# Optimization experiments

Measured on AMD Instinct MI355X. Metric: run time of the kernel, lower is better.

Reference implementation:

```python
import jax, jax.numpy as jnp
import numpy as np

# SpargeAttn / spas_sage2_attn_meansim block sizes
BLKQ, BLKK = 128, 64
NUM_HEADS = 8
SIMTHRESHD1 = 0.6
CDFTHRESHD = 0.98


def _block_meta(t, blk):
    # t: [B,H,S,D] -> block means [B,H,nb,D] and min-cosine-to-mean per block [B,H,nb]
    B, H, S, D = t.shape
    nb = S // blk
    tb = t.reshape(B, H, nb, blk, D)
    m = tb.mean(axis=3)
    tn = tb / (jnp.linalg.norm(tb, axis=-1, keepdims=True) + 1e-6)
    mn = m / (jnp.linalg.norm(m, axis=-1, keepdims=True) + 1e-6)
    cos = jnp.einsum('bhnkd,bhnd->bhnk', tn, mn)
    return m, cos.min(axis=-1)


def _meansim_sparse_attention(q, k, v, scale):
    # Block-sparse attention with mean-similarity pruning (SpargeAttn meansim).
    qm, qsim = _block_meta(q, BLKQ)          # [B,H,nq,D], [B,H,nq]
    km, ksim = _block_meta(k, BLKK)          # [B,H,nk,D], [B,H,nk]
    q_self = qsim > SIMTHRESHD1              # self-similar Q blocks -> mean is representative
    k_self = ksim > SIMTHRESHD1
    # pooled attention map over block means
    pooled = jax.nn.softmax(jnp.einsum('bhqd,bhkd->bhqk', qm, km) * scale, axis=-1)
    # per Q-block row: keep highest-prob K blocks until cumulative mass >= cdfthreshd
    order = jnp.argsort(-pooled, axis=-1)
    sp = jnp.take_along_axis(pooled, order, axis=-1)
    csum = jnp.cumsum(sp, axis=-1)
    keep_sorted = (csum - sp) < CDFTHRESHD   # always keeps at least the top block
    inv = jnp.argsort(order, axis=-1)
    keep = jnp.take_along_axis(keep_sorted, inv, axis=-1)  # [B,H,nq,nk]
    # conservative fallback: non-self-similar Q/K blocks are never pruned
    block_mask = keep | (~q_self)[..., None] | (~k_self)[:, :, None, :]
    tok_mask = jnp.repeat(jnp.repeat(block_mask, BLKQ, axis=2), BLKK, axis=3)
    s = jnp.einsum('bhqd,bhkd->bhqk', q, k) * scale
    s = jnp.where(tok_mask, s, -jnp.inf)
    p = jax.nn.softmax(s, axis=-1)
    return jnp.einsum('bhqk,bhkd->bhqd', p, v)


def setup_inputs() -> dict:
    key = jax.random.key(0)
    B, L, C = 2, 2048, 512
    ks = jax.random.split(key, 3)
    x = jax.random.normal(ks[0], (B, L, C), jnp.float32)
    Wqkv = jax.random.normal(ks[1], (C, 3 * C), jnp.float32) * (C ** -0.5)
    bqkv = jnp.zeros((3 * C,), jnp.float32)
    Wproj = jax.random.normal(ks[2], (C, C), jnp.float32) * (C ** -0.5)
    bproj = jnp.zeros((C,), jnp.float32)
    return {"x": x, "Wqkv": Wqkv, "bqkv": bqkv, "Wproj": Wproj, "bproj": bproj}


def reference(x, Wqkv, bqkv, Wproj, bproj):
    B, L, C = x.shape
    H = NUM_HEADS
    D = C // H
    scale = D ** -0.5
    qkv = (x @ Wqkv + bqkv).reshape(B, L, 3, H, D)
    qkv = jnp.transpose(qkv, (2, 0, 3, 1, 4))  # [3,B,H,L,D]
    q, k, v = qkv[0], qkv[1], qkv[2]
    o = _meansim_sparse_attention(q, k, v, scale)  # [B,H,L,D]
    o = jnp.transpose(o, (0, 2, 1, 3)).reshape(B, L, C)
    return o @ Wproj + bproj
```

## Files before the change

### kernel.cpp

```cpp
#include <hip/hip_runtime.h>
#include <math.h>

typedef unsigned short ushortT;
typedef unsigned int uintT;
typedef __attribute__((ext_vector_type(8))) short short8;
typedef __attribute__((ext_vector_type(16))) float f32x16;
#define MFMA32(a, b, c) __builtin_amdgcn_mfma_f32_32x32x16_bf16((a), (b), (c), 0, 0, 0)


#define LOG2E 1.4426950408889634f

static __device__ __forceinline__ ushortT f2b(float f) {
    union { float f; uintT u; } v; v.f = f;
    uintT u = v.u;
    u += 0x7fffu + ((u >> 16) & 1u);
    return (ushortT)(u >> 16);
}
static __device__ __forceinline__ uintT pack2(float a, float b) {
    return (uintT)f2b(a) | ((uintT)f2b(b) << 16);
}
static __device__ __forceinline__ uintT pack2t(float a, float b) {
    union { float f; uintT u; } x0, x1; x0.f = a; x1.f = b;
    return __builtin_amdgcn_perm(x1.u, x0.u, 0x07060302u);
}
static __device__ __forceinline__ float blo(uintT u) {
    union { uintT u; float f; } v; v.u = u << 16; return v.f;
}
static __device__ __forceinline__ float bhi(uintT u) {
    union { uintT u; float f; } v; v.u = u & 0xffff0000u; return v.f;
}
static __device__ __forceinline__ f32x16 zero16() {
    f32x16 z;
    #pragma unroll
    for (int i = 0; i < 16; ++i) z[i] = 0.f;
    return z;
}

#define B_N 2
#define H_N 8
#define L_N 2048
#define NQB 16
#define NKB 32

__global__ __launch_bounds__(256) void prep_kernel(
    const float* __restrict__ x, ushortT* __restrict__ xb,
    const float* __restrict__ Wq, ushortT* __restrict__ Wqt,
    const float* __restrict__ Wp, ushortT* __restrict__ Wpt) {
    const int bid = blockIdx.x, t = threadIdx.x;
    __shared__ float tile[32][33];
    if (bid < 2048) {
        int i = (bid * 256 + t) * 4;
        float4 v = *(const float4*)(x + i);
        uint2 o; o.x = pack2(v.x, v.y); o.y = pack2(v.z, v.w);
        *(uint2*)(xb + i) = o;
        return;
    }
    const float* W; ushortT* Wt; int C, c0, r0;
    if (bid < 2816) {
        const int b = bid - 2048;
        W = Wq; Wt = Wqt; C = 1536;
        c0 = (b % 48) * 32; r0 = (b / 48) * 32;
    } else {
        const int b = bid - 2816;
        W = Wp; Wt = Wpt; C = 512;
        c0 = (b & 15) * 32; r0 = (b >> 4) * 32;
    }
    const int tx = t & 31, ty = t >> 5;
    #pragma unroll
    for (int i = 0; i < 4; ++i)
        tile[ty + 8 * i][tx] = W[(size_t)(r0 + ty + 8 * i) * C + c0 + tx];
    __syncthreads();
    #pragma unroll
    for (int i = 0; i < 4; ++i) {
        int rr = ty + 8 * i;
        Wt[(size_t)(c0 + rr) * 512 + r0 + tx] = f2b(tile[tx][rr]);
    }
}

__global__ __launch_bounds__(256) void qkv_gemm_kernel(
    const ushortT* __restrict__ xb, const ushortT* __restrict__ wt,
    const float* __restrict__ bias,
    ushortT* __restrict__ qb, ushortT* __restrict__ kbuf, ushortT* __restrict__ vt,
    float* __restrict__ qm, float* __restrict__ km) {
    __shared__ __align__(16) ushortT As[2][128 * 40];
    __shared__ __align__(16) ushortT Bs[2][64 * 40];
    __shared__ float sumbuf[4][64];
    const int t = threadIdx.x;
    const int l = t & 63, w = t >> 6;
    const int lm = l & 31, lh = l >> 5;
    const int rowbase = blockIdx.y * 128;
    const int colbase = blockIdx.x * 64;

    f32x16 acc[2];
    acc[0] = zero16(); acc[1] = zero16();

    const int r = t >> 1, half = t & 1;
    const ushortT* Ag = xb + (size_t)(rowbase + r) * 512 + half * 16;
    const int soA = r * 40 + half * 16;
    const int rb = t >> 2, q4 = t & 3;
    const ushortT* Bg = wt + (size_t)(colbase + rb) * 512 + q4 * 8;
    const int soB = rb * 40 + q4 * 8;

    uint4 a0, a1, b0;
    a0 = *(const uint4*)(Ag); a1 = *(const uint4*)(Ag + 8);
    b0 = *(const uint4*)(Bg);
    *(uint4*)(&As[0][soA]) = a0; *(uint4*)(&As[0][soA] + 8) = a1;
    *(uint4*)(&Bs[0][soB]) = b0;

    for (int k0 = 0; k0 < 512; k0 += 32) {
        const int cur = (k0 >> 5) & 1;
        __syncthreads();
        if (k0 < 480) {
            a0 = *(const uint4*)(Ag + k0 + 32); a1 = *(const uint4*)(Ag + k0 + 40);
            b0 = *(const uint4*)(Bg + k0 + 32);
        }
        #pragma unroll
        for (int ks = 0; ks < 2; ++ks) {
            const int ko = 16 * ks + 8 * lh;
            short8 af  = *(const short8*)(&As[cur][(32 * w + lm) * 40 + ko]);
            short8 b_0 = *(const short8*)(&Bs[cur][lm * 40 + ko]);
            short8 b_1 = *(const short8*)(&Bs[cur][(32 + lm) * 40 + ko]);
            acc[0] = MFMA32(af, b_0, acc[0]);
            acc[1] = MFMA32(af, b_1, acc[1]);
        }
        if (k0 < 480) {
            const int nxt = cur ^ 1;
            *(uint4*)(&As[nxt][soA]) = a0; *(uint4*)(&As[nxt][soA] + 8) = a1;
            *(uint4*)(&Bs[nxt][soB]) = b0;
        }
    }

    const int which = blockIdx.x >> 3;
    const int h = blockIdx.x & 7;
    const int by = blockIdx.y;
    const int b = by >> 4;
    const size_t hb = (size_t)(b * 8 + h);
    float bias2[2];
    #pragma unroll
    for (int nt = 0; nt < 2; ++nt) bias2[nt] = bias[colbase + 32 * nt + lm];
    float msum[2] = {0.f, 0.f};
    #pragma unroll
    for (int nt = 0; nt < 2; ++nt) {
        const int dd = 32 * nt + lm;
        #pragma unroll
        for (int rg = 0; rg < 16; ++rg) {
            const int row_local = 32 * w + (rg & 3) + 8 * (rg >> 2) + 4 * lh;
            const int ll = (rowbase + row_local) & 2047;
            float val = acc[nt][rg] + bias2[nt];
            if (which == 0) {
                val *= 0.125f;
                msum[nt] += val;
                qb[(hb * 2048 + ll) * 64 + dd] = f2b(val * LOG2E);
            } else if (which == 1) {
                msum[nt] += val;
                kbuf[(hb * 2048 + ll) * 64 + dd] = f2b(val);
            } else {
                vt[hb * 131072 + (size_t)(ll >> 6) * 4096 + dd * 64 + (ll & 63)] = f2b(val);
            }
        }
    }
    if (which == 2) return;
    #pragma unroll
    for (int nt = 0; nt < 2; ++nt) {
        float s = msum[nt] + __shfl_xor(msum[nt], 32);
        if (l < 32) sumbuf[w][32 * nt + lm] = s;
    }
    __syncthreads();
    if (which == 0) {
        if (t < 64) {
            const int qbi = by & 15;
            qm[(hb * 16 + qbi) * 64 + t] =
                (sumbuf[0][t] + sumbuf[1][t] + sumbuf[2][t] + sumbuf[3][t]) * (1.0f / 128.0f);
        }
    } else {
        if (t < 128) {
            const int d = t & 63, pair = t >> 6;
            const int kbi = 2 * (by & 15) + pair;
            km[(hb * 32 + kbi) * 64 + d] =
                (sumbuf[2 * pair][d] + sumbuf[2 * pair + 1][d]) * (1.0f / 64.0f);
        }
    }
}

__global__ __launch_bounds__(256) void cos_kernel(const ushortT* __restrict__ qb,
                                                  const ushortT* __restrict__ kbuf,
                                                  const float* __restrict__ qm,
                                                  const float* __restrict__ km,
                                                  float* __restrict__ qs,
                                                  float* __restrict__ ks) {
    const int bh = blockIdx.y, t = threadIdx.x;
    const int l = t & 63, w = t >> 6;
    __shared__ float mS[64];
    __shared__ float wmin[4];
    if (blockIdx.z == 0) {
        if (blockIdx.x >= 16) return;
        const int qbk = blockIdx.x;
        if (t < 64) mS[t] = qm[((size_t)bh * 16 + qbk) * 64 + t];
        __syncthreads();
        float qn = 0.f;
        #pragma unroll
        for (int d = 0; d < 64; ++d) qn += mS[d] * mS[d];
        qn = sqrtf(qn);
        const int tok = t >> 1, half = t & 1;
        const ushortT* qrow = qb + ((size_t)bh * 2048 + qbk * 128 + tok) * 64 + half * 32;
        float dot = 0.f, nn = 0.f;
        #pragma unroll
        for (int c = 0; c < 4; ++c) {
            uint4 u = *(const uint4*)(qrow + c * 8);
            const int db = half * 32 + c * 8;
            float f0 = blo(u.x), f1 = bhi(u.x), f2 = blo(u.y), f3 = bhi(u.y);
            float f4 = blo(u.z), f5 = bhi(u.z), f6 = blo(u.w), f7 = bhi(u.w);
            dot += f0 * mS[db] + f1 * mS[db + 1] + f2 * mS[db + 2] + f3 * mS[db + 3]
                 + f4 * mS[db + 4] + f5 * mS[db + 5] + f6 * mS[db + 6] + f7 * mS[db + 7];
            nn += f0 * f0 + f1 * f1 + f2 * f2 + f3 * f3 + f4 * f4 + f5 * f5 + f6 * f6 + f7 * f7;
        }
        dot += __shfl_xor(dot, 1);
        nn += __shfl_xor(nn, 1);
        float cosv = dot / ((sqrtf(nn) + 1e-6f) * (qn + 1e-6f));
        #pragma unroll
        for (int off = 1; off < 64; off <<= 1) cosv = fminf(cosv, __shfl_xor(cosv, off));
        if (l == 0) wmin[w] = cosv;
        __syncthreads();
        if (t == 0)
            qs[bh * 16 + qbk] = fminf(fminf(wmin[0], wmin[1]), fminf(wmin[2], wmin[3]));
    } else {
        const int kbk = blockIdx.x;
        if (t < 64) mS[t] = km[((size_t)bh * 32 + kbk) * 64 + t];
        __syncthreads();
        float kn = 0.f;
        #pragma unroll
        for (int d = 0; d < 64; ++d) kn += mS[d] * mS[d];
        kn = sqrtf(kn);
        const int tok = t >> 2, quarter = t & 3;
        const ushortT* krow = kbuf + ((size_t)bh * 2048 + kbk * 64 + tok) * 64 + quarter * 16;
        float dot = 0.f, nn = 0.f;
        #pragma unroll
        for (int c = 0; c < 2; ++c) {
            uint4 u = *(const uint4*)(krow + c * 8);
            const int db = quarter * 16 + c * 8;
            float f0 = blo(u.x), f1 = bhi(u.x), f2 = blo(u.y), f3 = bhi(u.y);
            float f4 = blo(u.z), f5 = bhi(u.z), f6 = blo(u.w), f7 = bhi(u.w);
            dot += f0 * mS[db] + f1 * mS[db + 1] + f2 * mS[db + 2] + f3 * mS[db + 3]
                 + f4 * mS[db + 4] + f5 * mS[db + 5] + f6 * mS[db + 6] + f7 * mS[db + 7];
            nn += f0 * f0 + f1 * f1 + f2 * f2 + f3 * f3 + f4 * f4 + f5 * f5 + f6 * f6 + f7 * f7;
        }
        dot += __shfl_xor(dot, 1); dot += __shfl_xor(dot, 2);
        nn += __shfl_xor(nn, 1); nn += __shfl_xor(nn, 2);
        float cosv = dot / ((sqrtf(nn) + 1e-6f) * (kn + 1e-6f));
        #pragma unroll
        for (int off = 1; off < 64; off <<= 1) cosv = fminf(cosv, __shfl_xor(cosv, off));
        if (l == 0) wmin[w] = cosv;
        __syncthreads();
        if (t == 0)
            ks[bh * 32 + kbk] = fminf(fminf(wmin[0], wmin[1]), fminf(wmin[2], wmin[3]));
    }
}

__global__ __launch_bounds__(512) void mask_kernel(const float* __restrict__ qm,
                                                   const float* __restrict__ km,
                                                   const float* __restrict__ qs,
                                                   const float* __restrict__ ks,
                                                   int* __restrict__ maskp) {
    const int bh = blockIdx.x, t = threadIdx.x;
    __shared__ float qmS[16 * 64];
    __shared__ float kmS[32 * 64];
    __shared__ float pooled[16 * 32];
    __shared__ float pnorm[16 * 32];
    for (int i = t; i < 1024; i += 512) qmS[i] = qm[(size_t)bh * 1024 + i];
    for (int i = t; i < 2048; i += 512) kmS[i] = km[(size_t)bh * 2048 + i];
    __syncthreads();
    {
        const int qbi = t >> 5, kbi = t & 31;
        float dot = 0.f;
        #pragma unroll
        for (int d = 0; d < 64; ++d) dot += qmS[qbi * 64 + d] * kmS[kbi * 64 + d];
        pooled[t] = dot;
    }
    __syncthreads();
    if (t < 16) {
        float mx = -1e30f;
        #pragma unroll
        for (int kb = 0; kb < NKB; ++kb) mx = fmaxf(mx, pooled[t * 32 + kb]);
        float sum = 0.f;
        #pragma unroll
        for (int kb = 0; kb < NKB; ++kb) {
            const float e = expf(pooled[t * 32 + kb] - mx);
            pnorm[t * 32 + kb] = e;
            sum += e;
        }
        const float inv = 1.0f / sum;
        #pragma unroll
        for (int kb = 0; kb < NKB; ++kb) pnorm[t * 32 + kb] *= inv;
    }
    __syncthreads();
    {
        const int row = t >> 5, kb = t & 31;
        const float pk = pnorm[row * 32 + kb];
        float before = 0.f;
        #pragma unroll
        for (int j = 0; j < NKB; ++j) {
            const float pj = pnorm[row * 32 + j];
            if (pj > pk || (pj == pk && j < kb)) before += pj;
        }
        const bool keep = before < 0.98f;
        const bool qfb = !(qs[bh * 16 + row] > 0.6f);
        const bool kfb = !(ks[bh * 32 + kb] > 0.6f);
        maskp[((size_t)bh * 16 + row) * 32 + kb] = (keep || qfb || kfb) ? 1 : 0;
    }
}

#define KS_SH (128 * 72)
#define VS_SH (64 * 136)
__global__ __launch_bounds__(512, 2) void attn_kernel(
    const ushortT* __restrict__ qb, const ushortT* __restrict__ kbuf,
    const ushortT* __restrict__ vt, const int* __restrict__ maskp,
    ushortT* __restrict__ ob) {
    __shared__ __align__(16) ushortT smem[2 * KS_SH + 2 * VS_SH];
    __shared__ int klist[33];
    ushortT (*Ks)[KS_SH] = (ushortT(*)[KS_SH])smem;
    ushortT (*Vs)[VS_SH] = (ushortT(*)[VS_SH])(smem + 2 * KS_SH);

    const int t = threadIdx.x;
    const int l = t & 63, w = t >> 6;
    const int lm = l & 31, lh = l >> 5;
    const int qc = w >> 2, kq = w & 3;
    const int bh = blockIdx.x, qt = blockIdx.y;

    if (w == 0) {
        const int* mrow = maskp + ((size_t)bh * 16 + qt) * 32;
        const int keep = (l < 32) ? mrow[l] : 0;
        unsigned long long bal = __ballot(keep != 0);
        if (keep) {
            const int rank = __popcll(bal & ((1ULL << l) - 1ULL));
            klist[rank] = l;
        }
        if (l == 0) klist[32] = __popcll(bal);
    }
    const ushortT* qg = qb + ((size_t)bh * 2048 + qt * 128) * 64;
    short8 qf[4][2];
    #pragma unroll
    for (int qh = 0; qh < 2; ++qh)
        #pragma unroll
        for (int ksd = 0; ksd < 4; ++ksd)
            qf[ksd][qh] = *(const short8*)(qg + (64 * qc + 32 * qh + lm) * 64 + 16 * ksd + 8 * lh);
    __syncthreads();

    const int cnt = klist[32];
    const int nIter = (cnt + 1) >> 1;

    const int tile = t >> 7, tt = t & 127;
    const int isV = tile >> 1, skh = tile & 1;
    const int srow = tt >> 1, shalf = (tt & 1) * 32;
    const ushortT* gsrc = (isV ? vt : kbuf) + (size_t)bh * 131072;
    const int goff = srow * 64 + shalf;
    const int soff = isV ? (srow * 136 + skh * 64 + shalf)
                         : ((skh * 64 + srow) * 72 + shalf);
    ushortT* sd0 = (isV ? &Vs[0][soff] : &Ks[0][soff]);
    ushortT* sd1 = (isV ? &Vs[1][soff] : &Ks[1][soff]);

    f32x16 oacc[2][2];
    oacc[0][0] = zero16(); oacc[1][0] = zero16();
    oacc[0][1] = zero16(); oacc[1][1] = zero16();
    float l_i[2] = {0.f, 0.f};

    uint4 st0, st1, st2, st3;
    {
        int kidx = skh; if (kidx >= cnt) kidx = cnt - 1;
        const ushortT* g = gsrc + (size_t)klist[kidx] * 4096 + goff;
        st0 = *(const uint4*)(g);      st1 = *(const uint4*)(g + 8);
        st2 = *(const uint4*)(g + 16); st3 = *(const uint4*)(g + 24);
        *(uint4*)(sd0)      = st0; *(uint4*)(sd0 + 8)  = st1;
        *(uint4*)(sd0 + 16) = st2; *(uint4*)(sd0 + 24) = st3;
    }

    for (int i = 0; i < nIter; ++i) {
        const int cur = i & 1;
        __syncthreads();
        if (i + 1 < nIter) {
            int kidx = 2 * (i + 1) + skh; if (kidx >= cnt) kidx = cnt - 1;
            const ushortT* g = gsrc + (size_t)klist[kidx] * 4096 + goff;
            st0 = *(const uint4*)(g);      st1 = *(const uint4*)(g + 8);
            st2 = *(const uint4*)(g + 16); st3 = *(const uint4*)(g + 24);
        }
        const float mf = (2 * i + (kq >> 1) < cnt) ? 1.f : 0.f;
        f32x16 sacc[2];
        sacc[0] = zero16(); sacc[1] = zero16();
        #pragma unroll
        for (int ksd = 0; ksd < 4; ++ksd) {
            const int ko = 16 * ksd + 8 * lh;
            short8 kf = *(const short8*)(&Ks[cur][(32 * kq + lm) * 72 + ko]);
            sacc[0] = MFMA32(kf, qf[ksd][0], sacc[0]);
            sacc[1] = MFMA32(kf, qf[ksd][1], sacc[1]);
        }
        uintT uu[2][4][2];
        #pragma unroll
        for (int qh = 0; qh < 2; ++qh) {
            float psum0 = 0.f, psum1 = 0.f;
            #pragma unroll
            for (int rp = 0; rp < 8; ++rp) {
                const float e0 = __builtin_amdgcn_exp2f(sacc[qh][2 * rp]) * mf;
                const float e1 = __builtin_amdgcn_exp2f(sacc[qh][2 * rp + 1]) * mf;
                psum0 += e0; psum1 += e1;
                uu[qh][rp >> 1][rp & 1] = pack2t(e0, e1);
            }
            float psum = psum0 + psum1;
            psum += __shfl_xor(psum, 32);
            l_i[qh] += psum;
        }
        #pragma unroll
        for (int ksk = 0; ksk < 2; ++ksk) {
            const int vko = 32 * kq + 16 * ksk + 8 * lh;
            short8 vf0 = *(const short8*)(&Vs[cur][lm * 136 + vko]);
            short8 vf1 = *(const short8*)(&Vs[cur][(32 + lm) * 136 + vko]);
            #pragma unroll
            for (int qh = 0; qh < 2; ++qh) {
                const uintT kA = lh ? uu[qh][2 * ksk + 1][0] : uu[qh][2 * ksk][0];
                const uintT kB = lh ? uu[qh][2 * ksk + 1][1] : uu[qh][2 * ksk][1];
                const uintT sA = lh ? uu[qh][2 * ksk][0] : uu[qh][2 * ksk + 1][0];
                const uintT sB = lh ? uu[qh][2 * ksk][1] : uu[qh][2 * ksk + 1][1];
                const uintT rA = (uintT)__shfl_xor((int)sA, 32);
                const uintT rB = (uintT)__shfl_xor((int)sB, 32);
                union { uintT u[4]; short8 v; } cv;
                if (lh == 0) { cv.u[0] = kA; cv.u[1] = kB; cv.u[2] = rA; cv.u[3] = rB; }
                else         { cv.u[0] = rA; cv.u[1] = rB; cv.u[2] = kA; cv.u[3] = kB; }
                oacc[0][qh] = MFMA32(vf0, cv.v, oacc[0][qh]);
                oacc[1][qh] = MFMA32(vf1, cv.v, oacc[1][qh]);
            }
        }
        if (i + 1 < nIter) {
            ushortT* sd = (cur ^ 1) ? sd1 : sd0;
            *(uint4*)(sd)      = st0; *(uint4*)(sd + 8)  = st1;
            *(uint4*)(sd + 16) = st2; *(uint4*)(sd + 24) = st3;
        }
    }

    uint4* ox = (uint4*)smem;
    float* lx = (float*)((char*)smem + 49152);
    __syncthreads();
    if (kq != 0) {
        const int wslot = qc * 3 + (kq - 1);
        #pragma unroll
        for (int dt = 0; dt < 2; ++dt)
            #pragma unroll
            for (int qh = 0; qh < 2; ++qh)
                #pragma unroll
                for (int g2 = 0; g2 < 2; ++g2) {
                    uint4 u;
                    u.x = pack2(oacc[dt][qh][8 * g2 + 0], oacc[dt][qh][8 * g2 + 1]);
                    u.y = pack2(oacc[dt][qh][8 * g2 + 2], oacc[dt][qh][8 * g2 + 3]);
                    u.z = pack2(oacc[dt][qh][8 * g2 + 4], oacc[dt][qh][8 * g2 + 5]);
                    u.w = pack2(oacc[dt][qh][8 * g2 + 6], oacc[dt][qh][8 * g2 + 7]);
                    ox[(wslot * 8 + (dt * 4 + qh * 2 + g2)) * 64 + l] = u;
                }
        if (lh == 0) {
            lx[(wslot * 2 + 0) * 32 + lm] = l_i[0];
            lx[(wslot * 2 + 1) * 32 + lm] = l_i[1];
        }
    }
    __syncthreads();
    if (kq == 0) {
        float lt[2] = {l_i[0], l_i[1]};
        #pragma unroll
        for (int p = 0; p < 3; ++p) {
            const int ws2 = qc * 3 + p;
            lt[0] += lx[(ws2 * 2 + 0) * 32 + lm];
            lt[1] += lx[(ws2 * 2 + 1) * 32 + lm];
            #pragma unroll
            for (int dt = 0; dt < 2; ++dt)
                #pragma unroll
                for (int qh = 0; qh < 2; ++qh)
                    #pragma unroll
                    for (int g2 = 0; g2 < 2; ++g2) {
                        uint4 u = ox[(ws2 * 8 + (dt * 4 + qh * 2 + g2)) * 64 + l];
                        oacc[dt][qh][8 * g2 + 0] += blo(u.x);
                        oacc[dt][qh][8 * g2 + 1] += bhi(u.x);
                        oacc[dt][qh][8 * g2 + 2] += blo(u.y);
                        oacc[dt][qh][8 * g2 + 3] += bhi(u.y);
                        oacc[dt][qh][8 * g2 + 4] += blo(u.z);
                        oacc[dt][qh][8 * g2 + 5] += bhi(u.z);
                        oacc[dt][qh][8 * g2 + 6] += blo(u.w);
                        oacc[dt][qh][8 * g2 + 7] += bhi(u.w);
                    }
        }
        #pragma unroll
        for (int qh = 0; qh < 2; ++qh) {
            const float inv = 1.0f / lt[qh];
            const int token = qt * 128 + qc * 64 + 32 * qh + lm;
            ushortT* orow = ob + ((size_t)bh * 2048 + token) * 64;
            #pragma unroll
            for (int dt = 0; dt < 2; ++dt)
                #pragma unroll
                for (int rp = 0; rp < 8; ++rp) {
                    const int d0 = 32 * dt + 8 * (rp >> 1) + 4 * lh + 2 * (rp & 1);
                    *(uintT*)(orow + d0) =
                        pack2(oacc[dt][qh][2 * rp] * inv, oacc[dt][qh][2 * rp + 1] * inv);
                }
        }
    }
}

__global__ __launch_bounds__(256) void proj_gemm_kernel(
    const ushortT* __restrict__ ob, const ushortT* __restrict__ wpt,
    const float* __restrict__ bias, float* __restrict__ out) {
    __shared__ __align__(16) ushortT As[2][64 * 40];
    __shared__ __align__(16) ushortT Bs[2][64 * 40];
    const int t = threadIdx.x;
    const int l = t & 63, w = t >> 6;
    const int lm = l & 31, lh = l >> 5;
    const int rh = w & 1, ch = w >> 1;
    const int rowbase = blockIdx.y * 64;
    const int colbase = blockIdx.x * 64;

    f32x16 acc = zero16();

    const int r = t >> 2, q4 = t & 3;
    const int token = rowbase + r;
    const int b2 = token >> 11, lt = token & 2047;
    const int so = r * 40 + q4 * 8;
    const ushortT* obbase = ob + ((size_t)(b2 * 8) * 2048 + lt) * 64 + q4 * 8;
    const ushortT* Bg = wpt + (size_t)(colbase + r) * 512 + q4 * 8;

    uint4 a0, b0;
    a0 = *(const uint4*)(obbase);
    b0 = *(const uint4*)(Bg);
    *(uint4*)(&As[0][so]) = a0;
    *(uint4*)(&Bs[0][so]) = b0;

    for (int k0 = 0; k0 < 512; k0 += 32) {
        const int cur = (k0 >> 5) & 1;
        __syncthreads();
        if (k0 < 480) {
            const int kn = k0 + 32;
            const ushortT* Ag = obbase + (size_t)(kn >> 6) * 131072 + (kn & 63);
            a0 = *(const uint4*)(Ag);
            b0 = *(const uint4*)(Bg + kn);
        }
        #pragma unroll
        for (int ks = 0; ks < 2; ++ks) {
            const int ko = 16 * ks + 8 * lh;
            short8 af = *(const short8*)(&As[cur][(32 * rh + lm) * 40 + ko]);
            short8 bf = *(const short8*)(&Bs[cur][(32 * ch + lm) * 40 + ko]);
            acc = MFMA32(af, bf, acc);
        }
        if (k0 < 480) {
            const int nxt = cur ^ 1;
            *(uint4*)(&As[nxt][so]) = a0;
            *(uint4*)(&Bs[nxt][so]) = b0;
        }
    }
    const int c = colbase + 32 * ch + lm;
    const float bb = bias[c];
    #pragma unroll
    for (int rg = 0; rg < 16; ++rg) {
        const int row_local = 32 * rh + (rg & 3) + 8 * (rg >> 2) + 4 * lh;
        out[(size_t)(rowbase + row_local) * 512 + c] = acc[rg] + bb;
    }
}

extern "C" void kernel_launch(void* const* d_in, const int* in_sizes, int n_in,
                              void* d_out, int out_size, void* d_ws, size_t ws_size,
                              hipStream_t stream) {
    const float* x     = (const float*)d_in[0];
    const float* Wqkv  = (const float*)d_in[1];
    const float* bqkv  = (const float*)d_in[2];
    const float* Wproj = (const float*)d_in[3];
    const float* bproj = (const float*)d_in[4];
    float* out = (float*)d_out;

    char* w = (char*)d_ws;
    ushortT* xb     = (ushortT*)(w);
    ushortT* wqkvt  = (ushortT*)(w + 4194304);
    ushortT* wprojt = (ushortT*)(w + 5767168);
    ushortT* qb     = (ushortT*)(w + 6291456);
    ushortT* kbuf   = (ushortT*)(w + 10485760);
    ushortT* vt     = (ushortT*)(w + 14680064);
    ushortT* ob     = (ushortT*)(w + 18874368);
    float*   qm     = (float*)(w + 23068672);
    float*   km     = (float*)(w + 23134208);
    int*     maskp  = (int*)(w + 23265280);
    float*   qs     = (float*)(w + 36406272);
    float*   ks     = (float*)(w + 36407296);

    prep_kernel<<<3072, 256, 0, stream>>>(x, xb, Wqkv, wqkvt, Wproj, wprojt);
    qkv_gemm_kernel<<<dim3(24, 32), 256, 0, stream>>>(xb, wqkvt, bqkv, qb, kbuf, vt, qm, km);
    cos_kernel<<<dim3(32, 16, 2), 256, 0, stream>>>(qb, kbuf, qm, km, qs, ks);
    mask_kernel<<<16, 512, 0, stream>>>(qm, km, qs, ks, maskp);
    attn_kernel<<<dim3(16, 16), 512, 0, stream>>>(qb, kbuf, vt, maskp, ob);
    proj_gemm_kernel<<<dim3(8, 64), 256, 0, stream>>>(ob, wprojt, bproj, out);
}
```

Measured before the change: 141.3 us.

## Drop LDS staging of K/V in attention; each wave reads its K blocks from global

Removes the double-buffered shared-memory staging of K and V tiles and the per-iteration block-wide barrier. Each wave now takes a strided subset of the kept K blocks (j = kq, kq+4, ...) and loads its K and V MFMA fragments straight from global memory, processing both 32-row halves of each 64-key block itself. This drops LDS traffic and synchronisation and shrinks shared memory to the reduction buffers, but fragment loads now come uncoalesced from global/L2 with no prefetch overlap, and work may be unbalanced across waves when the kept-block count is not a multiple of four.

```diff
diff --git a/kernel.cpp b/kernel.cpp
--- a/kernel.cpp
+++ b/kernel.cpp
@@ -309,16 +309,13 @@
     }
 }
 
-#define KS_SH (128 * 72)
-#define VS_SH (64 * 136)
 __global__ __launch_bounds__(512, 2) void attn_kernel(
     const ushortT* __restrict__ qb, const ushortT* __restrict__ kbuf,
     const ushortT* __restrict__ vt, const int* __restrict__ maskp,
     ushortT* __restrict__ ob) {
-    __shared__ __align__(16) ushortT smem[2 * KS_SH + 2 * VS_SH];
+    __shared__ __align__(16) uint4 ox[6 * 8 * 64];
+    __shared__ float lx[6 * 2 * 32];
     __shared__ int klist[33];
-    ushortT (*Ks)[KS_SH] = (ushortT(*)[KS_SH])smem;
-    ushortT (*Vs)[VS_SH] = (ushortT(*)[VS_SH])(smem + 2 * KS_SH);
 
     const int t = threadIdx.x;
     const int l = t & 63, w = t >> 6;
@@ -346,97 +343,66 @@
     __syncthreads();
 
     const int cnt = klist[32];
-    const int nIter = (cnt + 1) >> 1;
-
-    const int tile = t >> 7, tt = t & 127;
-    const int isV = tile >> 1, skh = tile & 1;
-    const int srow = tt >> 1, shalf = (tt & 1) * 32;
-    const ushortT* gsrc = (isV ? vt : kbuf) + (size_t)bh * 131072;
-    const int goff = srow * 64 + shalf;
-    const int soff = isV ? (srow * 136 + skh * 64 + shalf)
-                         : ((skh * 64 + srow) * 72 + shalf);
-    ushortT* sd0 = (isV ? &Vs[0][soff] : &Ks[0][soff]);
-    ushortT* sd1 = (isV ? &Vs[1][soff] : &Ks[1][soff]);
+    const ushortT* kgb = kbuf + (size_t)bh * 131072;
+    const ushortT* vgb = vt + (size_t)bh * 131072;
 
     f32x16 oacc[2][2];
     oacc[0][0] = zero16(); oacc[1][0] = zero16();
     oacc[0][1] = zero16(); oacc[1][1] = zero16();
     float l_i[2] = {0.f, 0.f};
 
-    uint4 st0, st1, st2, st3;
-    {
-        int kidx = skh; if (kidx >= cnt) kidx = cnt - 1;
-        const ushortT* g = gsrc + (size_t)klist[kidx] * 4096 + goff;
-        st0 = *(const uint4*)(g);      st1 = *(const uint4*)(g + 8);
-        st2 = *(const uint4*)(g + 16); st3 = *(const uint4*)(g + 24);
-        *(uint4*)(sd0)      = st0; *(uint4*)(sd0 + 8)  = st1;
-        *(uint4*)(sd0 + 16) = st2; *(uint4*)(sd0 + 24) = st3;
-    }
-
-    for (int i = 0; i < nIter; ++i) {
-        const int cur = i & 1;
-        __syncthreads();
-        if (i + 1 < nIter) {
-            int kidx = 2 * (i + 1) + skh; if (kidx >= cnt) kidx = cnt - 1;
-            const ushortT* g = gsrc + (size_t)klist[kidx] * 4096 + goff;
-            st0 = *(const uint4*)(g);      st1 = *(const uint4*)(g + 8);
-            st2 = *(const uint4*)(g + 16); st3 = *(const uint4*)(g + 24);
-        }
-        const float mf = (2 * i + (kq >> 1) < cnt) ? 1.f : 0.f;
-        f32x16 sacc[2];
-        sacc[0] = zero16(); sacc[1] = zero16();
-        #pragma unroll
-        for (int ksd = 0; ksd < 4; ++ksd) {
-            const int ko = 16 * ksd + 8 * lh;
-            short8 kf = *(const short8*)(&Ks[cur][(32 * kq + lm) * 72 + ko]);
-            sacc[0] = MFMA32(kf, qf[ksd][0], sacc[0]);
-            sacc[1] = MFMA32(kf, qf[ksd][1], sacc[1]);
-        }
-        uintT uu[2][4][2];
-        #pragma unroll
-        for (int qh = 0; qh < 2; ++qh) {
-            float psum0 = 0.f, psum1 = 0.f;
+    for (int j = kq; j < cnt; j += 4) {
+        const int kb = klist[j];
+        const ushortT* kg = kgb + (size_t)kb * 4096;
+        const ushortT* vg = vgb + (size_t)kb * 4096;
+        #pragma unroll
+        for (int kh = 0; kh < 2; ++kh) {
+            f32x16 sacc[2];
+            sacc[0] = zero16(); sacc[1] = zero16();
             #pragma unroll
-            for (int rp = 0; rp < 8; ++rp) {
-                const float e0 = __builtin_amdgcn_exp2f(sacc[qh][2 * rp]) * mf;
-                const float e1 = __builtin_amdgcn_exp2f(sacc[qh][2 * rp + 1]) * mf;
-                psum0 += e0; psum1 += e1;
-                uu[qh][rp >> 1][rp & 1] = pack2t(e0, e1);
+            for (int ksd = 0; ksd < 4; ++ksd) {
+                short8 kf = *(const short8*)(kg + (32 * kh + lm) * 64 + 16 * ksd + 8 * lh);
+                sacc[0] = MFMA32(kf, qf[ksd][0], sacc[0]);
+                sacc[1] = MFMA32(kf, qf[ksd][1], sacc[1]);
             }
-            float psum = psum0 + psum1;
-            psum += __shfl_xor(psum, 32);
-            l_i[qh] += psum;
-        }
-        #pragma unroll
-        for (int ksk = 0; ksk < 2; ++ksk) {
-            const int vko = 32 * kq + 16 * ksk + 8 * lh;
-            short8 vf0 = *(const short8*)(&Vs[cur][lm * 136 + vko]);
-            short8 vf1 = *(const short8*)(&Vs[cur][(32 + lm) * 136 + vko]);
+            uintT uu[2][4][2];
             #pragma unroll
             for (int qh = 0; qh < 2; ++qh) {
-                const uintT kA = lh ? uu[qh][2 * ksk + 1][0] : uu[qh][2 * ksk][0];
-                const uintT kB = lh ? uu[qh][2 * ksk + 1][1] : uu[qh][2 * ksk][1];
-                const uintT sA = lh ? uu[qh][2 * ksk][0] : uu[qh][2 * ksk + 1][0];
-                const uintT sB = lh ? uu[qh][2 * ksk][1] : uu[qh][2 * ksk + 1][1];
-                const uintT rA = (uintT)__shfl_xor((int)sA, 32);
-                const uintT rB = (uintT)__shfl_xor((int)sB, 32);
-                union { uintT u[4]; short8 v; } cv;
-                if (lh == 0) { cv.u[0] = kA; cv.u[1] = kB; cv.u[2] = rA; cv.u[3] = rB; }
-                else         { cv.u[0] = rA; cv.u[1] = rB; cv.u[2] = kA; cv.u[3] = kB; }
-                oacc[0][qh] = MFMA32(vf0, cv.v, oacc[0][qh]);
-                oacc[1][qh] = MFMA32(vf1, cv.v, oacc[1][qh]);
+                float psum0 = 0.f, psum1 = 0.f;
+                #pragma unroll
+                for (int rp = 0; rp < 8; ++rp) {
+                    const float e0 = __builtin_amdgcn_exp2f(sacc[qh][2 * rp]);
+                    const float e1 = __builtin_amdgcn_exp2f(sacc[qh][2 * rp + 1]);
+                    psum0 += e0; psum1 += e1;
+                    uu[qh][rp >> 1][rp & 1] = pack2t(e0, e1);
+                }
+                float psum = psum0 + psum1;
+                psum += __shfl_xor(psum, 32);
+                l_i[qh] += psum;
             }
-        }
-        if (i + 1 < nIter) {
-            ushortT* sd = (cur ^ 1) ? sd1 : sd0;
-            *(uint4*)(sd)      = st0; *(uint4*)(sd + 8)  = st1;
-            *(uint4*)(sd + 16) = st2; *(uint4*)(sd + 24) = st3;
-        }
-    }
-
-    uint4* ox = (uint4*)smem;
-    float* lx = (float*)((char*)smem + 49152);
-    __syncthreads();
+            #pragma unroll
+            for (int ksk = 0; ksk < 2; ++ksk) {
+                const int vko = 32 * kh + 16 * ksk + 8 * lh;
+                short8 vf0 = *(const short8*)(vg + lm * 64 + vko);
+                short8 vf1 = *(const short8*)(vg + (32 + lm) * 64 + vko);
+                #pragma unroll
+                for (int qh = 0; qh < 2; ++qh) {
+                    const uintT kA = lh ? uu[qh][2 * ksk + 1][0] : uu[qh][2 * ksk][0];
+                    const uintT kB = lh ? uu[qh][2 * ksk + 1][1] : uu[qh][2 * ksk][1];
+                    const uintT sA = lh ? uu[qh][2 * ksk][0] : uu[qh][2 * ksk + 1][0];
+                    const uintT sB = lh ? uu[qh][2 * ksk][1] : uu[qh][2 * ksk + 1][1];
+                    const uintT rA = (uintT)__shfl_xor((int)sA, 32);
+                    const uintT rB = (uintT)__shfl_xor((int)sB, 32);
+                    union { uintT u[4]; short8 v; } cv;
+                    if (lh == 0) { cv.u[0] = kA; cv.u[1] = kB; cv.u[2] = rA; cv.u[3] = rB; }
+                    else         { cv.u[0] = rA; cv.u[1] = rB; cv.u[2] = kA; cv.u[3] = kB; }
+                    oacc[0][qh] = MFMA32(vf0, cv.v, oacc[0][qh]);
+                    oacc[1][qh] = MFMA32(vf1, cv.v, oacc[1][qh]);
+                }
+            }
+        }
+    }
+
     if (kq != 0) {
         const int wslot = qc * 3 + (kq - 1);
         #pragma unroll
```

Result: slower. 149.9 us (+6.1%).

## Fuse cosine-similarity into QKV GEMM epilogue and mask into attention prologue

Applied to the files above, without the earlier changes.

The per-block min-cosine computation moves into the QKV GEMM epilogue, working on the fp32 accumulators already in registers. This removes the separate cos_kernel launch and its reread of Q/K from memory. The pooled softmax, CDF pruning and mask building move into the attention kernel prologue, one row per workgroup, which removes mask_kernel and the mask buffer. The cost is two fewer launches and less global traffic, traded for extra shuffle reductions in the GEMM epilogue and a small serial prologue in attention. Cosines now use unrounded fp32 values instead of bf16, which could flip threshold decisions slightly.

```diff
diff --git a/kernel.cpp b/kernel.cpp
--- a/kernel.cpp
+++ b/kernel.cpp
@@ -81,10 +81,13 @@
     const ushortT* __restrict__ xb, const ushortT* __restrict__ wt,
     const float* __restrict__ bias,
     ushortT* __restrict__ qb, ushortT* __restrict__ kbuf, ushortT* __restrict__ vt,
-    float* __restrict__ qm, float* __restrict__ km) {
+    float* __restrict__ qm, float* __restrict__ km,
+    float* __restrict__ qs, float* __restrict__ ks) {
     __shared__ __align__(16) ushortT As[2][128 * 40];
     __shared__ __align__(16) ushortT Bs[2][64 * 40];
     __shared__ float sumbuf[4][64];
+    __shared__ float meanS[2][64];
+    __shared__ float wminS[4];
     const int t = threadIdx.x;
     const int l = t & 63, w = t >> 6;
     const int lm = l & 31, lh = l >> 5;
@@ -115,8 +118,8 @@
             b0 = *(const uint4*)(Bg + k0 + 32);
         }
         #pragma unroll
-        for (int ks = 0; ks < 2; ++ks) {
-            const int ko = 16 * ks + 8 * lh;
+        for (int ks2 = 0; ks2 < 2; ++ks2) {
+            const int ko = 16 * ks2 + 8 * lh;
             short8 af  = *(const short8*)(&As[cur][(32 * w + lm) * 40 + ko]);
             short8 b_0 = *(const short8*)(&Bs[cur][lm * 40 + ko]);
             short8 b_1 = *(const short8*)(&Bs[cur][(32 + lm) * 40 + ko]);
@@ -157,6 +160,7 @@
             } else {
                 vt[hb * 131072 + (size_t)(ll >> 6) * 4096 + dd * 64 + (ll & 63)] = f2b(val);
             }
+            acc[nt][rg] = val;
         }
     }
     if (which == 2) return;
@@ -169,143 +173,54 @@
     if (which == 0) {
         if (t < 64) {
             const int qbi = by & 15;
-            qm[(hb * 16 + qbi) * 64 + t] =
+            const float m =
                 (sumbuf[0][t] + sumbuf[1][t] + sumbuf[2][t] + sumbuf[3][t]) * (1.0f / 128.0f);
+            qm[(hb * 16 + qbi) * 64 + t] = m;
+            meanS[0][t] = m;
         }
     } else {
         if (t < 128) {
             const int d = t & 63, pair = t >> 6;
             const int kbi = 2 * (by & 15) + pair;
-            km[(hb * 32 + kbi) * 64 + d] =
+            const float m =
                 (sumbuf[2 * pair][d] + sumbuf[2 * pair + 1][d]) * (1.0f / 64.0f);
-        }
-    }
-}
-
-__global__ __launch_bounds__(256) void cos_kernel(const ushortT* __restrict__ qb,
-                                                  const ushortT* __restrict__ kbuf,
-                                                  const float* __restrict__ qm,
-                                                  const float* __restrict__ km,
-                                                  float* __restrict__ qs,
-                                                  float* __restrict__ ks) {
-    const int bh = blockIdx.y, t = threadIdx.x;
-    const int l = t & 63, w = t >> 6;
-    __shared__ float mS[64];
-    __shared__ float wmin[4];
-    if (blockIdx.z == 0) {
-        if (blockIdx.x >= 16) return;
-        const int qbk = blockIdx.x;
-        if (t < 64) mS[t] = qm[((size_t)bh * 16 + qbk) * 64 + t];
-        __syncthreads();
-        float qn = 0.f;
-        #pragma unroll
-        for (int d = 0; d < 64; ++d) qn += mS[d] * mS[d];
-        qn = sqrtf(qn);
-        const int tok = t >> 1, half = t & 1;
-        const ushortT* qrow = qb + ((size_t)bh * 2048 + qbk * 128 + tok) * 64 + half * 32;
-        float dot = 0.f, nn = 0.f;
-        #pragma unroll
-        for (int c = 0; c < 4; ++c) {
-            uint4 u = *(const uint4*)(qrow + c * 8);
-            const int db = half * 32 + c * 8;
-            float f0 = blo(u.x), f1 = bhi(u.x), f2 = blo(u.y), f3 = bhi(u.y);
-            float f4 = blo(u.z), f5 = bhi(u.z), f6 = blo(u.w), f7 = bhi(u.w);
-            dot += f0 * mS[db] + f1 * mS[db + 1] + f2 * mS[db + 2] + f3 * mS[db + 3]
-                 + f4 * mS[db + 4] + f5 * mS[db + 5] + f6 * mS[db + 6] + f7 * mS[db + 7];
-            nn += f0 * f0 + f1 * f1 + f2 * f2 + f3 * f3 + f4 * f4 + f5 * f5 + f6 * f6 + f7 * f7;
-        }
-        dot += __shfl_xor(dot, 1);
-        nn += __shfl_xor(nn, 1);
-        float cosv = dot / ((sqrtf(nn) + 1e-6f) * (qn + 1e-6f));
-        #pragma unroll
-        for (int off = 1; off < 64; off <<= 1) cosv = fminf(cosv, __shfl_xor(cosv, off));
-        if (l == 0) wmin[w] = cosv;
-        __syncthreads();
-        if (t == 0)
-            qs[bh * 16 + qbk] = fminf(fminf(wmin[0], wmin[1]), fminf(wmin[2], wmin[3]));
-    } else {
-        const int kbk = blockIdx.x;
-        if (t < 64) mS[t] = km[((size_t)bh * 32 + kbk) * 64 + t];
-        __syncthreads();
-        float kn = 0.f;
-        #pragma unroll
-        for (int d = 0; d < 64; ++d) kn += mS[d] * mS[d];
-        kn = sqrtf(kn);
-        const int tok = t >> 2, quarter = t & 3;
-        const ushortT* krow = kbuf + ((size_t)bh * 2048 + kbk * 64 + tok) * 64 + quarter * 16;
-        float dot = 0.f, nn = 0.f;
-        #pragma unroll
-        for (int c = 0; c < 2; ++c) {
-            uint4 u = *(const uint4*)(krow + c * 8);
-            const int db = quarter * 16 + c * 8;
-            float f0 = blo(u.x), f1 = bhi(u.x), f2 = blo(u.y), f3 = bhi(u.y);
-            float f4 = blo(u.z), f5 = bhi(u.z), f6 = blo(u.w), f7 = bhi(u.w);
-            dot += f0 * mS[db] + f1 * mS[db + 1] + f2 * mS[db + 2] + f3 * mS[db + 3]
-                 + f4 * mS[db + 4] + f5 * mS[db + 5] + f6 * mS[db + 6] + f7 * mS[db + 7];
-            nn += f0 * f0 + f1 * f1 + f2 * f2 + f3 * f3 + f4 * f4 + f5 * f5 + f6 * f6 + f7 * f7;
-        }
-        dot += __shfl_xor(dot, 1); dot += __shfl_xor(dot, 2);
-        nn += __shfl_xor(nn, 1); nn += __shfl_xor(nn, 2);
-        float cosv = dot / ((sqrtf(nn) + 1e-6f) * (kn + 1e-6f));
-        #pragma unroll
-        for (int off = 1; off < 64; off <<= 1) cosv = fminf(cosv, __shfl_xor(cosv, off));
-        if (l == 0) wmin[w] = cosv;
-        __syncthreads();
-        if (t == 0)
-            ks[bh * 32 + kbk] = fminf(fminf(wmin[0], wmin[1]), fminf(wmin[2], wmin[3]));
-    }
-}
-
-__global__ __launch_bounds__(512) void mask_kernel(const float* __restrict__ qm,
-                                                   const float* __restrict__ km,
-                                                   const float* __restrict__ qs,
-                                                   const float* __restrict__ ks,
-                                                   int* __restrict__ maskp) {
-    const int bh = blockIdx.x, t = threadIdx.x;
-    __shared__ float qmS[16 * 64];
-    __shared__ float kmS[32 * 64];
-    __shared__ float pooled[16 * 32];
-    __shared__ float pnorm[16 * 32];
-    for (int i = t; i < 1024; i += 512) qmS[i] = qm[(size_t)bh * 1024 + i];
-    for (int i = t; i < 2048; i += 512) kmS[i] = km[(size_t)bh * 2048 + i];
+            km[(hb * 32 + kbi) * 64 + d] = m;
+            meanS[pair][d] = m;
+        }
+    }
     __syncthreads();
     {
-        const int qbi = t >> 5, kbi = t & 31;
-        float dot = 0.f;
-        #pragma unroll
-        for (int d = 0; d < 64; ++d) dot += qmS[qbi * 64 + d] * kmS[kbi * 64 + d];
-        pooled[t] = dot;
-    }
-    __syncthreads();
-    if (t < 16) {
-        float mx = -1e30f;
-        #pragma unroll
-        for (int kb = 0; kb < NKB; ++kb) mx = fmaxf(mx, pooled[t * 32 + kb]);
-        float sum = 0.f;
-        #pragma unroll
-        for (int kb = 0; kb < NKB; ++kb) {
-            const float e = expf(pooled[t * 32 + kb] - mx);
-            pnorm[t * 32 + kb] = e;
-            sum += e;
-        }
-        const float inv = 1.0f / sum;
-        #pragma unroll
-        for (int kb = 0; kb < NKB; ++kb) pnorm[t * 32 + kb] *= inv;
-    }
-    __syncthreads();
-    {
-        const int row = t >> 5, kb = t & 31;
-        const float pk = pnorm[row * 32 + kb];
-        float before = 0.f;
-        #pragma unroll
-        for (int j = 0; j < NKB; ++j) {
-            const float pj = pnorm[row * 32 + j];
-            if (pj > pk || (pj == pk && j < kb)) before += pj;
-        }
-        const bool keep = before < 0.98f;
-        const bool qfb = !(qs[bh * 16 + row] > 0.6f);
-        const bool kfb = !(ks[bh * 32 + kb] > 0.6f);
-        maskp[((size_t)bh * 16 + row) * 32 + kb] = (keep || qfb || kfb) ? 1 : 0;
+        const int mrow = (which == 0) ? 0 : (w >> 1);
+        const float mv0 = meanS[mrow][lm], mv1 = meanS[mrow][32 + lm];
+        float mn2 = mv0 * mv0 + mv1 * mv1;
+        #pragma unroll
+        for (int off = 1; off < 32; off <<= 1) mn2 += __shfl_xor(mn2, off);
+        const float mnorm = sqrtf(mn2);
+        float cmin = 1e30f;
+        #pragma unroll
+        for (int rg = 0; rg < 16; ++rg) {
+            float dp = acc[0][rg] * mv0 + acc[1][rg] * mv1;
+            float nn = acc[0][rg] * acc[0][rg] + acc[1][rg] * acc[1][rg];
+            #pragma unroll
+            for (int off = 1; off < 32; off <<= 1) {
+                dp += __shfl_xor(dp, off);
+                nn += __shfl_xor(nn, off);
+            }
+            const float cosv = dp / ((sqrtf(nn) + 1e-6f) * (mnorm + 1e-6f));
+            cmin = fminf(cmin, cosv);
+        }
+        cmin = fminf(cmin, __shfl_xor(cmin, 32));
+        if (l == 0) wminS[w] = cmin;
+    }
+    __syncthreads();
+    if (t == 0) {
+        if (which == 0) {
+            qs[hb * 16 + (by & 15)] =
+                fminf(fminf(wminS[0], wminS[1]), fminf(wminS[2], wminS[3]));
+        } else {
+            ks[hb * 32 + 2 * (by & 15)]     = fminf(wminS[0], wminS[1]);
+            ks[hb * 32 + 2 * (by & 15) + 1] = fminf(wminS[2], wminS[3]);
+        }
     }
 }
 
@@ -313,10 +228,14 @@
 #define VS_SH (64 * 136)
 __global__ __launch_bounds__(512, 2) void attn_kernel(
     const ushortT* __restrict__ qb, const ushortT* __restrict__ kbuf,
-    const ushortT* __restrict__ vt, const int* __restrict__ maskp,
+    const ushortT* __restrict__ vt,
+    const float* __restrict__ qm, const float* __restrict__ km,
+    const float* __restrict__ qs, const float* __restrict__ ks,
     ushortT* __restrict__ ob) {
     __shared__ __align__(16) ushortT smem[2 * KS_SH + 2 * VS_SH];
     __shared__ int klist[33];
+    __shared__ float qmS[64];
+    __shared__ float pnS[32];
     ushortT (*Ks)[KS_SH] = (ushortT(*)[KS_SH])smem;
     ushortT (*Vs)[VS_SH] = (ushortT(*)[VS_SH])(smem + 2 * KS_SH);
 
@@ -326,23 +245,47 @@
     const int qc = w >> 2, kq = w & 3;
     const int bh = blockIdx.x, qt = blockIdx.y;
 
-    if (w == 0) {
-        const int* mrow = maskp + ((size_t)bh * 16 + qt) * 32;
-        const int keep = (l < 32) ? mrow[l] : 0;
-        unsigned long long bal = __ballot(keep != 0);
+    if (t < 64) qmS[t] = qm[((size_t)bh * 16 + qt) * 64 + t];
+
+    const ushortT* qg = qb + ((size_t)bh * 2048 + qt * 128) * 64;
+    short8 qf[4][2];
+    #pragma unroll
+    for (int qh = 0; qh < 2; ++qh)
+        #pragma unroll
+        for (int ksd = 0; ksd < 4; ++ksd)
+            qf[ksd][qh] = *(const short8*)(qg + (64 * qc + 32 * qh + lm) * 64 + 16 * ksd + 8 * lh);
+    __syncthreads();
+
+    if (w == 0 && l < 32) {
+        const float* kmr = km + ((size_t)bh * 32 + l) * 64;
+        float dot = 0.f;
+        #pragma unroll
+        for (int d = 0; d < 64; ++d) dot += qmS[d] * kmr[d];
+        float mx = dot;
+        #pragma unroll
+        for (int off = 1; off < 32; off <<= 1) mx = fmaxf(mx, __shfl_xor(mx, off));
+        const float e = expf(dot - mx);
+        float sum = e;
+        #pragma unroll
+        for (int off = 1; off < 32; off <<= 1) sum += __shfl_xor(sum, off);
+        const float pn = e * (1.0f / sum);
+        pnS[l] = pn;
+        float before = 0.f;
+        #pragma unroll
+        for (int j = 0; j < 32; ++j) {
+            const float pj = pnS[j];
+            if (pj > pn || (pj == pn && j < l)) before += pj;
+        }
+        const bool qfb = !(qs[bh * 16 + qt] > 0.6f);
+        const bool kfb = !(ks[bh * 32 + l] > 0.6f);
+        const bool keep = (before < 0.98f) || qfb || kfb;
+        unsigned long long bal = __ballot(keep);
         if (keep) {
             const int rank = __popcll(bal & ((1ULL << l) - 1ULL));
             klist[rank] = l;
         }
         if (l == 0) klist[32] = __popcll(bal);
     }
-    const ushortT* qg = qb + ((size_t)bh * 2048 + qt * 128) * 64;
-    short8 qf[4][2];
-    #pragma unroll
-    for (int qh = 0; qh < 2; ++qh)
-        #pragma unroll
-        for (int ksd = 0; ksd < 4; ++ksd)
-            qf[ksd][qh] = *(const short8*)(qg + (64 * qc + 32 * qh + lm) * 64 + 16 * ksd + 8 * lh);
     __syncthreads();
 
     const int cnt = klist[32];
@@ -536,8 +479,8 @@
             b0 = *(const uint4*)(Bg + kn);
         }
         #pragma unroll
-        for (int ks = 0; ks < 2; ++ks) {
-            const int ko = 16 * ks + 8 * lh;
+        for (int ks2 = 0; ks2 < 2; ++ks2) {
+            const int ko = 16 * ks2 + 8 * lh;
             short8 af = *(const short8*)(&As[cur][(32 * rh + lm) * 40 + ko]);
             short8 bf = *(const short8*)(&Bs[cur][(32 * ch + lm) * 40 + ko]);
             acc = MFMA32(af, bf, acc);
@@ -577,14 +520,12 @@
     ushortT* ob     = (ushortT*)(w + 18874368);
     float*   qm     = (float*)(w + 23068672);
     float*   km     = (float*)(w + 23134208);
-    int*     maskp  = (int*)(w + 23265280);
     float*   qs     = (float*)(w + 36406272);
     float*   ks     = (float*)(w + 36407296);
 
     prep_kernel<<<3072, 256, 0, stream>>>(x, xb, Wqkv, wqkvt, Wproj, wprojt);
-    qkv_gemm_kernel<<<dim3(24, 32), 256, 0, stream>>>(xb, wqkvt, bqkv, qb, kbuf, vt, qm, km);
-    cos_kernel<<<dim3(32, 16, 2), 256, 0, stream>>>(qb, kbuf, qm, km, qs, ks);
-    mask_kernel<<<16, 512, 0, stream>>>(qm, km, qs, ks, maskp);
-    attn_kernel<<<dim3(16, 16), 512, 0, stream>>>(qb, kbuf, vt, maskp, ob);
+    qkv_gemm_kernel<<<dim3(24, 32), 256, 0, stream>>>(xb, wqkvt, bqkv, qb, kbuf, vt,
+                                                      qm, km, qs, ks);
+    attn_kernel<<<dim3(16, 16), 512, 0, stream>>>(qb, kbuf, vt, qm, km, qs, ks, ob);
     proj_gemm_kernel<<<dim3(8, 64), 256, 0, stream>>>(ob, wprojt, bproj, out);
 }
```

New measurement: 135.4 us. 1.04x faster.
